# Optimization experiments

Measured on AMD Instinct MI355X. Metric: run time of the kernel, lower is better.

The kernel has to match this reference:

```python
import jax, jax.numpy as jnp
import numpy as np

B, T, N, C = 4, 6, 512, 8
HID, FEAT, EMB, IN_DIM = 64, 16, 32, 1
KS, KC, HORIZON = 3, 2, 3
ALPHA = 3.0

def _init(key, shape):
    fin = shape[-2] if len(shape) >= 2 else shape[-1]
    return jax.random.normal(key, shape, dtype=jnp.float32) * (1.0 / fin) ** 0.5

def setup_inputs():
    ks = jax.random.split(jax.random.key(0), 32)
    L_enc = (IN_DIM + FEAT + HID) * KS * KC
    L_dec = (HID + FEAT + HID) * KS * KC
    return {
        "X_seq": jax.random.normal(ks[0], (B, T, N, C), dtype=jnp.float32),
        "As": jax.random.uniform(ks[1], (N, N), dtype=jnp.float32) / N,
        "Ac": jax.random.uniform(ks[2], (C, C), dtype=jnp.float32) / C,
        "feature": jax.random.normal(ks[3], (N, FEAT), dtype=jnp.float32),
        "Wu_S": _init(ks[4], (C, HID)), "Wv_S": _init(ks[5], (C, HID)),
        "Wu_C": _init(ks[6], (N, HID)), "Wv_C": _init(ks[7], (N, HID)),
        "mfS_w1": _init(ks[8], (4, 2, 256)), "mfS_b1": jnp.zeros((4, 256), jnp.float32),
        "mfS_w2": _init(ks[9], (4, 256, 256)), "mfS_b2": jnp.zeros((4, 256), jnp.float32),
        "mfC_w1": _init(ks[10], (4, 2, 256)), "mfC_b1": jnp.zeros((4, 256), jnp.float32),
        "mfC_w2": _init(ks[11], (4, 256, 256)), "mfC_b2": jnp.zeros((4, 256), jnp.float32),
        "enc_gW": _init(ks[12], (L_enc, 2 * HID)), "enc_gb": jnp.zeros((2 * HID,), jnp.float32),
        "enc_cW": _init(ks[13], (L_enc, HID)), "enc_cb": jnp.zeros((HID,), jnp.float32),
        "dec_gW": _init(ks[14], (L_dec, 2 * HID)), "dec_gb": jnp.zeros((2 * HID,), jnp.float32),
        "dec_cW": _init(ks[15], (L_dec, HID)), "dec_cb": jnp.zeros((HID,), jnp.float32),
        "out_w1": _init(ks[16], (HID, EMB)), "out_b1": jnp.zeros((EMB,), jnp.float32),
        "out_w2": _init(ks[17], (EMB, IN_DIM)), "out_b2": jnp.zeros((IN_DIM,), jnp.float32),
    }

def _mlp(x, w1, b1, w2, b2):
    return jax.nn.relu(x @ w1 + b1) @ w2 + b2

def _mixed_fusion(A, P, w1, b1, w2, b2):
    # node_feat = [rowsum(A), rowsum(P)]; key/value MLPs indexed 0:key_A 1:key_P 2:val_A 3:val_P
    nf = jnp.stack([A.sum(-1), P.sum(-1)], axis=-1)            # [n, 2]
    An, Pn = A @ nf, P @ nf
    key = _mlp(An, w1[0], b1[0], w2[0], b2[0]) + _mlp(Pn, w1[1], b1[1], w2[1], b2[1])
    val = _mlp(An, w1[2], b1[2], w2[2], b2[2]) + _mlp(Pn, w1[3], b1[3], w2[3], b2[3])
    a = jax.nn.sigmoid(key @ val.T)
    return a * A + (1.0 - a) * P

def _adaptive_graph(Xf, Wu, Wv):
    U = jnp.tanh(ALPHA * Xf @ Wu)                              # [b,t,n,h]
    V = jnp.tanh(ALPHA * Xf @ Wv)
    M = jnp.einsum('btnh,btmh->nm', U, V)
    # Ps = softmax(relu(M - M^T)) matches einsum pair in torch source
    return jax.nn.softmax(jax.nn.relu(M - M.T), axis=-1)

def _cheby(G, K):
    mats = [jnp.eye(G.shape[0], dtype=G.dtype), G]
    for _ in range(2, K):
        mats.append(2.0 * G @ mats[-1] - mats[-2])
    return jnp.stack(mats[:K], axis=0)                         # [K, n, n]

def _bdg(X, Gs_set, Gc_set, W, b):
    # X: [b,n,c,l]; fused Ks x Kc Chebyshev mode products; cat order (k, j, l) matches torch cat
    t1 = jnp.einsum('bncl,knm->kbmcl', X, Gs_set)
    t2 = jnp.einsum('kbmcl,jcd->bmdkjl', t1, Gc_set)
    feat = t2.reshape(t2.shape[0], t2.shape[1], t2.shape[2], -1)
    return feat @ W + b

def _cell(Xt, Ht, featx, Gs_set, Gc_set, gW, gb, cW, cb):
    XH = jnp.concatenate([Xt, Ht, featx], axis=-1)
    uv = _bdg(XH, Gs_set, Gc_set, gW, gb)
    update = jax.nn.sigmoid(uv[..., :HID])
    reset = jax.nn.sigmoid(uv[..., HID:])
    cand_in = jnp.concatenate([Xt, reset * Ht, featx], axis=-1)
    cand = jnp.tanh(_bdg(cand_in, Gs_set, Gc_set, cW, cb))
    return (1.0 - update) * Ht + update * cand

def _forward(X_seq, As, Ac, feature, Wu_S, Wv_S, Wu_C, Wv_C,
             mfS_w1, mfS_b1, mfS_w2, mfS_b2, mfC_w1, mfC_b1, mfC_w2, mfC_b2,
             enc_gW, enc_gb, enc_cW, enc_cb, dec_gW, dec_gb, dec_cW, dec_cb,
             out_w1, out_b1, out_w2, out_b2):
    # MGP_Gen: adaptive spatial / categorical graphs fused with priors
    Ps = _adaptive_graph(X_seq, Wu_S, Wv_S)
    Gs = _mixed_fusion(As, Ps, mfS_w1, mfS_b1, mfS_w2, mfS_b2)
    Xc = jnp.swapaxes(X_seq, 2, 3)                             # [b,t,c,n]
    Pc = _adaptive_graph(Xc, Wu_C, Wv_C)
    Gc = _mixed_fusion(Ac, Pc, mfC_w1, mfC_b1, mfC_w2, mfC_b2)
    Gs_set, Gc_set = _cheby(Gs, KS), _cheby(Gc, KC)
    featx = jnp.broadcast_to(feature[None, :, None, :], (B, N, C, FEAT))
    X5 = X_seq[..., None]                                      # [b,t,n,c,1]
    Ht = jnp.zeros((B, N, C, HID), dtype=X_seq.dtype)
    for t in range(T):                                         # encoder GRU over history
        Ht = _cell(X5[:, t], Ht, featx, Gs_set, Gc_set, enc_gW, enc_gb, enc_cW, enc_cb)
    deco_in, Hd = Ht, Ht
    outs = []
    for _ in range(HORIZON):
        Hd = _cell(deco_in, Hd, featx, Gs_set, Gc_set, dec_gW, dec_gb, dec_cW, dec_cb)
        outs.append(_mlp(Hd, out_w1, out_b1, out_w2, out_b2))
        deco_in = Hd
    return jnp.stack(outs, axis=1)                             # [b, horizon, n, c, 1]

def reference(X_seq, As, Ac, feature, Wu_S, Wv_S, Wu_C, Wv_C, mfS_w1, mfS_b1, mfS_w2, mfS_b2, mfC_w1, mfC_b1, mfC_w2, mfC_b2, enc_gW, enc_gb, enc_cW, enc_cb, dec_gW, dec_gb, dec_cW, dec_cb, out_w1, out_b1, out_w2, out_b2):
    return _forward(X_seq, As, Ac, feature, Wu_S, Wv_S, Wu_C, Wv_C, mfS_w1, mfS_b1, mfS_w2, mfS_b2, mfC_w1, mfC_b1, mfC_w2, mfC_b2, enc_gW, enc_gb, enc_cW, enc_cb, dec_gW, dec_gb, dec_cW, dec_cb, out_w1, out_b1, out_w2, out_b2)
```

## Files before the change

### kernel.cpp

```cpp
#include <hip/hip_runtime.h>
#include <math.h>

constexpr int kB = 4, kT = 6, kN = 512, kC = 8;
constexpr int kH = 64, kF = 16, kE = 32;
constexpr int kKS = 3, kKC = 2, kHOR = 3;
constexpr int kBT = kB * kT;
constexpr int kRK = kBT * kH;
constexpr int L_ENC = 1 + kH + kF;
constexpr int L_DEC = kH + kH + kF;
constexpr int PL_ENC = 96;
constexpr int PL_DEC = 160;
constexpr int KP_ENC = 3 * PL_ENC;
constexpr int KP_DEC = 3 * PL_DEC;
constexpr float kALPHA = 3.0f;

typedef unsigned short ushortT;
typedef short short8 __attribute__((ext_vector_type(8)));
typedef float f32x4 __attribute__((ext_vector_type(4)));

__device__ __forceinline__ float sigm(float x) { return 1.0f / (1.0f + __expf(-x)); }

__device__ __forceinline__ ushortT f2bf(float f) {
    union { float f; unsigned int u; } v; v.f = f;
    unsigned int r = v.u + 0x7fffu + ((v.u >> 16) & 1u);
    return (ushortT)(r >> 16);
}

__device__ __forceinline__ void fma44(const float4& a, const float4& b, float acc[4][4]) {
    acc[0][0] += a.x*b.x; acc[0][1] += a.x*b.y; acc[0][2] += a.x*b.z; acc[0][3] += a.x*b.w;
    acc[1][0] += a.y*b.x; acc[1][1] += a.y*b.y; acc[1][2] += a.y*b.z; acc[1][3] += a.y*b.w;
    acc[2][0] += a.z*b.x; acc[2][1] += a.z*b.y; acc[2][2] += a.z*b.z; acc[2][3] += a.z*b.w;
    acc[3][0] += a.w*b.x; acc[3][1] += a.w*b.y; acc[3][2] += a.w*b.z; acc[3][3] += a.w*b.w;
}


__global__ __launch_bounds__(256) void k_uvproj_s(
    const float* __restrict__ X, const float* __restrict__ Wu, const float* __restrict__ Wv,
    float* __restrict__ Upr, float* __restrict__ Vpr)
{
    int idx = blockIdx.x * blockDim.x + threadIdx.x;
    if (idx >= kN * kBT * kH) return;
    int h = idx % kH; int bt = (idx / kH) % kBT; int n = idx / (kH * kBT);
    const float* xr = X + ((size_t)bt * kN + n) * kC;
    float u = 0.f, v = 0.f;
#pragma unroll
    for (int c = 0; c < kC; ++c) { float x = xr[c]; u += x * Wu[c*kH + h]; v += x * Wv[c*kH + h]; }
    Upr[(size_t)n * kRK + bt * kH + h] = tanhf(kALPHA * u);
    Vpr[(size_t)n * kRK + bt * kH + h] = tanhf(kALPHA * v);
}

__global__ __launch_bounds__(512) void k_uvproj_c2(
    const float* __restrict__ X, const float* __restrict__ WuC, const float* __restrict__ WvC,
    float* __restrict__ Uc, float* __restrict__ Vc)
{
    __shared__ float Xs[4096];
    __shared__ float Wus[4096], Wvs[4096];
    int bt = blockIdx.x, tid = threadIdx.x;
    for (int i = tid; i < 4096; i += 512) Xs[i] = X[(size_t)bt*4096 + i];
    int c = tid >> 6, h = tid & 63;
    float u = 0.f, v = 0.f;
    for (int n0 = 0; n0 < 512; n0 += 64) {
        __syncthreads();
        for (int i = tid; i < 4096; i += 512) { Wus[i] = WuC[n0*64 + i]; Wvs[i] = WvC[n0*64 + i]; }
        __syncthreads();
#pragma unroll 8
        for (int nn = 0; nn < 64; ++nn) {
            float x = Xs[(n0+nn)*8 + c];
// ... 178 lines not shown
    if (tid < 16) {
        int i = tid >> 1, comp = tid & 1;
        float an = 0.f, pn = 0.f;
#pragma unroll
        for (int j = 0; j < 8; ++j) {
            float nfj = comp ? 1.f : rsA[j];
            an += Ac[i*8+j] * nfj; pn += Pcs[i*8+j] * nfj;
        }
        Ans[i*2+comp] = an; Pns[i*2+comp] = pn;
    }
    __syncthreads();
    for (int e = tid; e < 2048; e += 256) {
        int i = e >> 8, o = e & 255;
        hA[i][o] = fmaxf(Ans[i*2]*w1[qa*512 + o] + Ans[i*2+1]*w1[qa*512 + 256 + o] + b1[qa*256 + o], 0.f);
        hP[i][o] = fmaxf(Pns[i*2]*w1[qp*512 + o] + Pns[i*2+1]*w1[qp*512 + 256 + o] + b1[qp*256 + o], 0.f);
    }
    __syncthreads();
    for (int e = tid; e < 512; e += 256) {
        int i = e >> 6, oc = c0 + (e & 63);
        float s = b2[qa*256 + oc] + b2[qp*256 + oc];
        for (int k = 0; k < 256; ++k)
            s += hA[i][k]*w2[(size_t)qa*65536 + k*256 + oc] + hP[i][k]*w2[(size_t)qp*65536 + k*256 + oc];
        keyval[(size_t)kv*2048 + i*256 + oc] = s;
    }
}

__global__ void k_gcfuse2(const float* __restrict__ keyval, const float* __restrict__ Mc,
                          const float* __restrict__ Ac, float* __restrict__ GcF)
{
    __shared__ float Pcs[64];
    int t = threadIdx.x; if (t >= 64) return;
    if (t < 8) {
        int i = t;
        float row[8]; float mx = -1e30f;
#pragma unroll
        for (int j = 0; j < 8; ++j) { float v = fmaxf(Mc[i*8+j] - Mc[j*8+i], 0.f); row[j] = v; mx = fmaxf(mx, v); }
        float s = 0.f;
#pragma unroll
        for (int j = 0; j < 8; ++j) { row[j] = __expf(row[j] - mx); s += row[j]; }
        float inv = 1.f / s;
#pragma unroll
        for (int j = 0; j < 8; ++j) Pcs[i*8+j] = row[j] * inv;
    }
    __syncthreads();
    int c = t >> 3, d = t & 7;
    const float* key = keyval;
    const float* val = keyval + 2048;
    float s = 0.f;
    for (int k = 0; k < 256; ++k) s += key[c*256 + k] * val[d*256 + k];
    float a = sigm(s);
    GcF[c*8 + d] = a*Ac[c*8 + d] + (1.f - a)*Pcs[c*8 + d];
}


__global__ void k_transp(const float* __restrict__ G, ushortT* __restrict__ Gt)
{
    __shared__ float tile[32][33];
    int bx = blockIdx.x * 32, by = blockIdx.y * 32;
    int x = threadIdx.x, y0 = threadIdx.y;
    for (int yy = y0; yy < 32; yy += 8) tile[yy][x] = G[(size_t)(by+yy)*kN + bx + x];
    __syncthreads();
    for (int yy = y0; yy < 32; yy += 8) Gt[(size_t)(bx+yy)*kN + by + x] = f2bf(tile[x][yy]);
}

__global__ __launch_bounds__(256) void k_prep_wt(
    const float* __restrict__ W, ushortT* __restrict__ WT,
    int L, int PL, int KP, int outW, int mode)
{
    int idx = blockIdx.x * blockDim.x + threadIdx.x;
    if (idx >= 2 * outW * KP) return;
    int qp = idx % KP, o = idx / KP;
    int kk = qp / PL, l = qp - kk * PL;
    int lo;
    if (mode == 1) lo = (l < 64) ? l + 1 : (l == 64) ? 0 : (l < 80) ? L : (l - 15);
    else lo = l;
    int j = o / outW, oo = o - j * outW;
    float v = (lo < L) ? W[(size_t)((kk*2 + j)*L + lo) * outW + oo] : 0.f;
    WT[idx] = f2bf(v);
}

__global__ __launch_bounds__(256) void k_cheby_mfma(
    const ushortT* __restrict__ Gst, ushortT* __restrict__ Gst2)
{
    __shared__ short sA[128][40];
    __shared__ short sB[128][40];
    int tid = threadIdx.x;
    int m0 = blockIdx.y * 128, j0 = blockIdx.x * 128;
    int w = tid >> 6, lane = tid & 63, wr = w >> 1, wc = w & 1;
    f32x4 acc[4][4];
#pragma unroll
    for (int i = 0; i < 4; ++i)
#pragma unroll
        for (int j = 0; j < 4; ++j) acc[i][j] = (f32x4){0.f, 0.f, 0.f, 0.f};
    for (int k0 = 0; k0 < kN; k0 += 32) {
        {
            int row = tid >> 1, lc = (tid & 1) * 16;
            const ushortT* p = Gst + (size_t)(m0 + row)*kN + k0 + lc;
            *(short8*)&sA[row][lc]     = *(const short8*)p;
            *(short8*)&sA[row][lc + 8] = *(const short8*)(p + 8);
        }
        {
            int kr = tid & 31, jc = (tid >> 5) * 8;
#pragma unroll
            for (int rep = 0; rep < 2; ++rep) {
                short8 v = *(const short8*)(Gst + (size_t)(k0 + kr)*kN + j0 + jc + rep*64);
#pragma unroll
                for (int i = 0; i < 8; ++i) sB[jc + rep*64 + i][kr] = v[i];
            }
        }
        __syncthreads();
        short8 af[4], bfr[4];
#pragma unroll
        for (int mi = 0; mi < 4; ++mi)
            af[mi] = *(const short8*)&sA[wr*64 + mi*16 + (lane & 15)][(lane >> 4) * 8];
#pragma unroll
        for (int ni = 0; ni < 4; ++ni)
            bfr[ni] = *(const short8*)&sB[wc*64 + ni*16 + (lane & 15)][(lane >> 4) * 8];
#pragma unroll
        for (int mi = 0; mi < 4; ++mi)
#pragma unroll
            for (int ni = 0; ni < 4; ++ni)
                acc[mi][ni] = __builtin_amdgcn_mfma_f32_16x16x32_bf16(af[mi], bfr[ni], acc[mi][ni], 0, 0, 0);
        __syncthreads();
    }
#pragma unroll
    for (int mi = 0; mi < 4; ++mi) {
#pragma unroll
        for (int ni = 0; ni < 4; ++ni) {
            int row0 = m0 + wr*64 + mi*16 + (lane >> 4) * 4;
            int col  = j0 + wc*64 + ni*16 + (lane & 15);
#pragma unroll
            for (int q = 0; q < 4; ++q) {
                int row = row0 + q;
                Gst2[(size_t)row*kN + col] = f2bf(2.f*acc[mi][ni][q] - (row == col ? 1.f : 0.f));
            }
        }
    }
}

template<int CLP, int PL, int ACTW, int OFF>
__global__ __launch_bounds__(256) void k_t1m(
    const ushortT* __restrict__ Gst, const ushortT* __restrict__ Xin, ushortT* __restrict__ Yout)
{
    __shared__ short sA[128][40];
    __shared__ short sB[128][40];
    int tid = threadIdx.x;
    int ki = blockIdx.z >> 2, b = blockIdx.z & 3;
    const ushortT* A = Gst + (size_t)ki * kN * kN;
    const ushortT* B = Xin + (size_t)b * kN * CLP;
    ushortT* C = Yout + (size_t)(ki*4 + b) * kN * CLP;
    int m0 = blockIdx.y * 128, j0 = blockIdx.x * 128;
    int w = tid >> 6, lane = tid & 63, wr = w >> 1, wc = w & 1;
    f32x4 acc[4][4];
#pragma unroll
    for (int i = 0; i < 4; ++i)
#pragma unroll
        for (int j = 0; j < 4; ++j) acc[i][j] = (f32x4){0.f, 0.f, 0.f, 0.f};

    for (int k0 = 0; k0 < kN; k0 += 32) {
        {
            int row = tid >> 1, lc = (tid & 1) * 16;
            const ushortT* p = A + (size_t)(m0 + row)*kN + k0 + lc;
            *(short8*)&sA[row][lc]     = *(const short8*)p;
            *(short8*)&sA[row][lc + 8] = *(const short8*)(p + 8);
        }
        {
            int kr = tid & 31, jc = (tid >> 5) * 8;
#pragma unroll
            for (int rep = 0; rep < 2; ++rep) {
                int j = j0 + jc + rep*64;
                int cg = j / ACTW;
                int col = cg*PL + OFF + (j - cg*ACTW);
                short8 v = *(const short8*)(B + (size_t)(k0 + kr)*CLP + col);
#pragma unroll
                for (int i = 0; i < 8; ++i) sB[jc + rep*64 + i][kr] = v[i];
            }
        }
        __syncthreads();
        short8 af[4], bfr[4];
#pragma unroll
        for (int mi = 0; mi < 4; ++mi)
            af[mi] = *(const short8*)&sA[wr*64 + mi*16 + (lane & 15)][(lane >> 4) * 8];
#pragma unroll
        for (int ni = 0; ni < 4; ++ni)
            bfr[ni] = *(const short8*)&sB[wc*64 + ni*16 + (lane & 15)][(lane >> 4) * 8];
#pragma unroll
        for (int mi = 0; mi < 4; ++mi)
#pragma unroll
            for (int ni = 0; ni < 4; ++ni)
                acc[mi][ni] = __builtin_amdgcn_mfma_f32_16x16x32_bf16(af[mi], bfr[ni], acc[mi][ni], 0, 0, 0);
        __syncthreads();
    }
#pragma unroll
    for (int mi = 0; mi < 4; ++mi) {
#pragma unroll
        for (int ni = 0; ni < 4; ++ni) {
            int row = m0 + wr*64 + mi*16 + (lane >> 4) * 4;
            int fj = j0 + wc*64 + ni*16;
            int cg = fj / ACTW;
            int col = cg*PL + OFF + (fj - cg*ACTW) + (lane & 15);
#pragma unroll
            for (int q = 0; q < 4; ++q)
                C[(size_t)(row + q)*CLP + col] = f2bf(acc[mi][ni][q]);
        }
    }
}

template<int PL, int KP, int XOFF>
__global__ __launch_bounds__(256) void k_gates_f(
    ushortT* __restrict__ XH, const ushortT* __restrict__ Yb,
    const ushortT* __restrict__ WT, const float* __restrict__ GcM,
    const float* __restrict__ gb, const float* __restrict__ Ht,
    float* __restrict__ upd)
{
    __shared__ short sA[64][40];
    __shared__ short sB[256][40];
    __shared__ float sEp[32][260];
    __shared__ float GcS[64], gbS[128];
    int tid = threadIdx.x;
    int r0 = blockIdx.x * 64;
    int b = r0 >> 12, rr = r0 & 4095;
    const ushortT* src0 = XH + (size_t)r0 * PL;
    const ushortT* src1 = Yb + ((size_t)b * 4096 + rr) * PL;
    const ushortT* src2 = Yb + ((size_t)(4 + b) * 4096 + rr) * PL;
    if (tid < 64) GcS[tid] = GcM[tid];
    if (tid >= 64 && tid < 192) gbS[tid - 64] = gb[tid - 64];
    int w = tid >> 6, lane = tid & 63;
    f32x4 acc[4][4];
#pragma unroll
    for (int i = 0; i < 4; ++i)
#pragma unroll
        for (int j = 0; j < 4; ++j) acc[i][j] = (f32x4){0.f, 0.f, 0.f, 0.f};

    for (int k0 = 0; k0 < KP; k0 += 32) {
        int kk = k0 / PL, l0 = k0 - kk * PL;
        const ushortT* Ap = (kk == 0) ? src0 : (kk == 1) ? src1 : src2;
        {
            int row = tid >> 2, lc = (tid & 3) * 8;
            *(short8*)&sA[row][lc] = *(const short8*)(Ap + (size_t)row*PL + l0 + lc);
        }
        {
            const ushortT* p = WT + (size_t)tid*KP + k0;
            *(short8*)&sB[tid][0]  = *(const short8*)(p);
            *(short8*)&sB[tid][8]  = *(const short8*)(p + 8);
            *(short8*)&sB[tid][16] = *(const short8*)(p + 16);
            *(short8*)&sB[tid][24] = *(const short8*)(p + 24);
        }
        __syncthreads();
        short8 af[4], bfr[4];
#pragma unroll
        for (int mi = 0; mi < 4; ++mi)
            af[mi] = *(const short8*)&sA[mi*16 + (lane & 15)][(lane >> 4) * 8];
#pragma unroll
        for (int ni = 0; ni < 4; ++ni)
            bfr[ni] = *(const short8*)&sB[w*64 + ni*16 + (lane & 15)][(lane >> 4) * 8];
#pragma unroll
        for (int mi = 0; mi < 4; ++mi)
#pragma unroll
            for (int ni = 0; ni < 4; ++ni)
                acc[mi][ni] = __builtin_amdgcn_mfma_f32_16x16x32_bf16(af[mi], bfr[ni], acc[mi][ni], 0, 0, 0);
        __syncthreads();
    }
    for (int chunk = 0; chunk < 2; ++chunk) {
#pragma unroll
        for (int mi2 = 0; mi2 < 2; ++mi2) {
            int mi = chunk*2 + mi2;
#pragma unroll
            for (int ni = 0; ni < 4; ++ni)
#pragma unroll
                for (int q = 0; q < 4; ++q)
                    sEp[mi2*16 + (lane >> 4)*4 + q][w*64 + ni*16 + (lane & 15)] = acc[mi][ni][q];
        }
        __syncthreads();
        for (int it = 0; it < 16; ++it) {
            int idx = it*256 + tid;
            int o = idx & 127, rloc = idx >> 7;
            int r = r0 + chunk*32 + rloc;
            int d = r & 7, bb = rloc & ~7;
            float pre = sEp[rloc][o] + gbS[o];
#pragma unroll
            for (int c = 0; c < 8; ++c) pre += GcS[c*8 + d] * sEp[bb + c][128 + o];
            float g = sigm(pre);
            if (o < 64) upd[(size_t)r*64 + o] = g;
            else {
                int h = o - 64;
                XH[(size_t)r*PL + XOFF + h] = f2bf(g * Ht[(size_t)r*64 + h]);
            }
        }
        __syncthreads();
    }
}

template<int PL, int KP>
__global__ __launch_bounds__(256) void k_cand_f(
    const ushortT* __restrict__ XH, const ushortT* __restrict__ Yb,
    const ushortT* __restrict__ WT, const float* __restrict__ GcM,
    const float* __restrict__ cb, const float* __restrict__ upd,
    float* __restrict__ Ht)
{
    __shared__ short sA[64][40];
    __shared__ short sB[128][40];
    __shared__ float sEp[64][132];
    __shared__ float GcS[64], cbS[64];
    int tid = threadIdx.x;
    int r0 = blockIdx.x * 64;
    int b = r0 >> 12, rr = r0 & 4095;
    const ushortT* src0 = XH + (size_t)r0 * PL;
    const ushortT* src1 = Yb + ((size_t)b * 4096 + rr) * PL;
    const ushortT* src2 = Yb + ((size_t)(4 + b) * 4096 + rr) * PL;
    if (tid < 64) GcS[tid] = GcM[tid];
    if (tid >= 64 && tid < 128) cbS[tid - 64] = cb[tid - 64];
    int w = tid >> 6, lane = tid & 63;
    f32x4 acc[4][2];
#pragma unroll
    for (int i = 0; i < 4; ++i)
#pragma unroll
        for (int j = 0; j < 2; ++j) acc[i][j] = (f32x4){0.f, 0.f, 0.f, 0.f};

    for (int k0 = 0; k0 < KP; k0 += 32) {
        int kk = k0 / PL, l0 = k0 - kk * PL;
        const ushortT* Ap = (kk == 0) ? src0 : (kk == 1) ? src1 : src2;
        {
            int row = tid >> 2, lc = (tid & 3) * 8;
            *(short8*)&sA[row][lc] = *(const short8*)(Ap + (size_t)row*PL + l0 + lc);
        }
        {
            int col = tid >> 1, seg = (tid & 1) * 16;
            const ushortT* p = WT + (size_t)col*KP + k0 + seg;
            *(short8*)&sB[col][seg]     = *(const short8*)p;
            *(short8*)&sB[col][seg + 8] = *(const short8*)(p + 8);
        }
        __syncthreads();
        short8 af[4], bfr[2];
#pragma unroll
        for (int mi = 0; mi < 4; ++mi)
            af[mi] = *(const short8*)&sA[mi*16 + (lane & 15)][(lane >> 4) * 8];
#pragma unroll
        for (int ni = 0; ni < 2; ++ni)
            bfr[ni] = *(const short8*)&sB[w*32 + ni*16 + (lane & 15)][(lane >> 4) * 8];
#pragma unroll
        for (int mi = 0; mi < 4; ++mi)
#pragma unroll
            for (int ni = 0; ni < 2; ++ni)
                acc[mi][ni] = __builtin_amdgcn_mfma_f32_16x16x32_bf16(af[mi], bfr[ni], acc[mi][ni], 0, 0, 0);
        __syncthreads();
    }
#pragma unroll
    for (int mi = 0; mi < 4; ++mi)
#pragma unroll
        for (int ni = 0; ni < 2; ++ni)
#pragma unroll
            for (int q = 0; q < 4; ++q)
                sEp[mi*16 + (lane >> 4)*4 + q][w*32 + ni*16 + (lane & 15)] = acc[mi][ni][q];
    __syncthreads();
    for (int it = 0; it < 16; ++it) {
        int idx = it*256 + tid;
        int o = idx & 63, rloc = idx >> 6;
        int r = r0 + rloc;
        int d = r & 7, bb = rloc & ~7;
        float pre = sEp[rloc][o] + cbS[o];
#pragma unroll
        for (int c = 0; c < 8; ++c) pre += GcS[c*8 + d] * sEp[bb + c][64 + o];
        float cv = tanhf(pre);
        float u = upd[(size_t)r*64 + o];
        float h0 = Ht[(size_t)r*64 + o];
        Ht[(size_t)r*64 + o] = (1.f - u)*h0 + u*cv;
    }
}


__global__ __launch_bounds__(256) void k_build_enc(
    const float* __restrict__ X, int t, const float* __restrict__ Ht,
    const float* __restrict__ featr, ushortT* __restrict__ XH)
{
    int idx = blockIdx.x * blockDim.x + threadIdx.x;
    if (idx >= 16384 * PL_ENC) return;
    int l = idx % PL_ENC; int r = idx / PL_ENC;
    int c = r & 7; int m = (r >> 3) & 511; int b = r >> 12;
    float v;
    if (l < 64)            v = Ht[(size_t)r*kH + l];
    else if (l == 64)      v = X[(((size_t)b*kT + t)*kN + m)*kC + c];
    else if (l < 80)       v = 0.f;
    else                   v = featr[m*kF + (l - 80)];
    XH[idx] = f2bf(v);
}

__global__ __launch_bounds__(256) void k_build_dec(
    const float* __restrict__ Ht, const float* __restrict__ featr, ushortT* __restrict__ XH)
{
    int idx = blockIdx.x * blockDim.x + threadIdx.x;
    if (idx >= 16384 * PL_DEC) return;
    int l = idx % PL_DEC; int r = idx / PL_DEC;
    int m = (r >> 3) & 511;
    float v;
    if (l < kH)            v = Ht[(size_t)r*kH + l];
    else if (l < 2*kH)     v = Ht[(size_t)r*kH + l - kH];
    else if (l < L_DEC)    v = featr[m*kF + l - 2*kH];
    else                   v = 0.f;
    XH[idx] = f2bf(v);
}

__global__ __launch_bounds__(256) void k_outmlp(
    const float* __restrict__ Hd, const float* __restrict__ w1, const float* __restrict__ b1,
    const float* __restrict__ w2, const float* __restrict__ b2, float* __restrict__ out, int hz)
{
    int idx = blockIdx.x * blockDim.x + threadIdx.x;
    if (idx >= kB*kN*kC) return;
    int c = idx % kC; int m = (idx / kC) % kN; int b = idx / (kC*kN);
    const float* h = Hd + (size_t)idx * kH;
    float hreg[kH];
#pragma unroll
    for (int k = 0; k < kH; ++k) hreg[k] = h[k];
    float acc = b2[0];
    for (int e = 0; e < kE; ++e) {
        float s = b1[e];
#pragma unroll
        for (int k = 0; k < kH; ++k) s += hreg[k] * w1[k*kE + e];
        acc += fmaxf(s, 0.f) * w2[e];
    }
    out[((size_t)(b*kHOR + hz)*kN + m)*kC + c] = acc;
}

extern "C" void kernel_launch(void* const* d_in, const int* in_sizes, int n_in,
                              void* d_out, int out_size, void* d_ws, size_t ws_size,
                              hipStream_t stream)
{
    (void)in_sizes; (void)n_in; (void)out_size; (void)ws_size;
    const float* X      = (const float*)d_in[0];
    const float* As     = (const float*)d_in[1];
    const float* Ac     = (const float*)d_in[2];
    const float* featr  = (const float*)d_in[3];
    const float* WuS    = (const float*)d_in[4];
    const float* WvS    = (const float*)d_in[5];
    const float* WuC    = (const float*)d_in[6];
    const float* WvC    = (const float*)d_in[7];
    const float* mfS_w1 = (const float*)d_in[8];
    const float* mfS_b1 = (const float*)d_in[9];
    const float* mfS_w2 = (const float*)d_in[10];
    const float* mfS_b2 = (const float*)d_in[11];
    const float* mfC_w1 = (const float*)d_in[12];
    const float* mfC_b1 = (const float*)d_in[13];
    const float* mfC_w2 = (const float*)d_in[14];
    const float* mfC_b2 = (const float*)d_in[15];
    const float* enc_gW = (const float*)d_in[16];
    const float* enc_gb = (const float*)d_in[17];
    const float* enc_cW = (const float*)d_in[18];
    const float* enc_cb = (const float*)d_in[19];
    const float* dec_gW = (const float*)d_in[20];
    const float* dec_gb = (const float*)d_in[21];
    const float* dec_cW = (const float*)d_in[22];
    const float* dec_cb = (const float*)d_in[23];
    const float* out_w1 = (const float*)d_in[24];
    const float* out_b1 = (const float*)d_in[25];
    const float* out_w2 = (const float*)d_in[26];
    const float* out_b2 = (const float*)d_in[27];
    float* out = (float*)d_out;
    float* ws = (float*)d_ws;

    float* Ht     = ws;
    float* updb   = Ht + 1048576;
    float* Gg     = updb + 1048576;
    float* Gs     = Gg + 4194304;
    float* smallf = Gs + 262144;
    float* nfS = smallf;
    float* AnS = nfS + 1024;
    float* PnS = AnS + 1024;
    float* McB = PnS + 1024;
    float* GcF = McB + 64;
    float* kvC = GcF + 64;
    ushortT* XHb  = (ushortT*)(smallf + 8192);
    ushortT* Yb   = XHb + 2621440;
    ushortT* GstB = Yb + 5242880;
    ushortT* WTg_e = GstB + 524288;
    ushortT* WTc_e = WTg_e + 73728;
    ushortT* WTg_d = WTc_e + 36864;
    ushortT* WTc_d = WTg_d + 122880;
    float* Upr   = Gg;
    float* Vpr   = Upr + 786432;
    float* part  = Vpr + 786432;
    float* Ms    = part + 1048576;
    float* Ps    = Ms + 262144;
    float* hidAP = Ps + 262144;
    float* keyS  = hidAP + 262144;
    float* valS  = keyS + 131072;
    float* w2tK  = valS + 131072;
    float* w2tV  = w2tK + 131072;
    float* Uc    = w2tV + 131072;
    float* Vc    = Uc + 12288;

    constexpr int CLP_ENC = kC * PL_ENC;
    constexpr int CLP_DEC = kC * PL_DEC;

    hipMemsetAsync(Ht, 0, (size_t)16384 * kH * sizeof(float), stream);

    k_prep_wt<<<(2*128*KP_ENC + 255)/256, 256, 0, stream>>>(enc_gW, WTg_e, L_ENC, PL_ENC, KP_ENC, 128, 1);
    k_prep_wt<<<(2*64 *KP_ENC + 255)/256, 256, 0, stream>>>(enc_cW, WTc_e, L_ENC, PL_ENC, KP_ENC, 64, 1);
    k_prep_wt<<<(2*128*KP_DEC + 255)/256, 256, 0, stream>>>(dec_gW, WTg_d, L_DEC, PL_DEC, KP_DEC, 128, 0);
    k_prep_wt<<<(2*64 *KP_DEC + 255)/256, 256, 0, stream>>>(dec_cW, WTc_d, L_DEC, PL_DEC, KP_DEC, 64, 0);
    k_prep_w2t<<<512, 256, 0, stream>>>(mfS_w2, w2tK, w2tV);

    k_uvproj_s<<<(kN*kBT*kH + 255)/256, 256, 0, stream>>>(X, WuS, WvS, Upr, Vpr);
    k_gemm_ntsk<<<dim3(8, 8, 4), 256, 0, stream>>>(Upr, Vpr, part, 512, 512, 1536, 384);
    k_redep<<<1024, 256, 0, stream>>>(part, 4, 262144, 512, Ms, 0, nullptr, nullptr);
    k_nfa<<<kN, 256, 0, stream>>>(As, nfS);
    k_softmax_anpn<<<kN, 256, 0, stream>>>(Ms, As, nfS, Ps, AnS, PnS);
    k_mlp1cat<<<1024, 256, 0, stream>>>(AnS, PnS, mfS_w1, mfS_b1, 0, 1, hidAP);
    k_gemm_ntsk<<<dim3(4, 8, 2), 256, 0, stream>>>(hidAP, w2tK, part, 512, 256, 512, 256);
    k_redep<<<512, 256, 0, stream>>>(part, 2, 131072, 256, keyS, 2, mfS_b2, mfS_b2 + 256);
    k_mlp1cat<<<1024, 256, 0, stream>>>(AnS, PnS, mfS_w1, mfS_b1, 2, 3, hidAP);
    k_gemm_ntsk<<<dim3(4, 8, 2), 256, 0, stream>>>(hidAP, w2tV, part, 512, 256, 512, 256);
    k_redep<<<512, 256, 0, stream>>>(part, 2, 131072, 256, valS, 2, mfS_b2 + 512, mfS_b2 + 768);
    k_gemm_ntsk<<<dim3(8, 8, 2), 256, 0, stream>>>(keyS, valS, part, 512, 512, 256, 128);
    k_redep<<<1024, 256, 0, stream>>>(part, 2, 262144, 512, Gs, 1, As, Ps);
    k_transp<<<dim3(16, 16), dim3(32, 8), 0, stream>>>(Gs, GstB);
    k_cheby_mfma<<<dim3(4, 4), 256, 0, stream>>>(GstB, GstB + 262144);

    k_uvproj_c2<<<kBT, 512, 0, stream>>>(X, WuC, WvC, Uc, Vc);
    k_mc2<<<1, 512, 0, stream>>>(Uc, Vc, McB);
    k_catmlp2<<<dim3(2, 4), 256, 0, stream>>>(McB, Ac, mfC_w1, mfC_b1, mfC_w2, mfC_b2, kvC);
    k_gcfuse2<<<1, 64, 0, stream>>>(kvC, McB, Ac, GcF);

    bool featDone = false;
    for (int t = 0; t < kT; ++t) {
        k_build_enc<<<(16384*PL_ENC + 255)/256, 256, 0, stream>>>(X, t, Ht, featr, XHb);
        if (!featDone) {
            k_t1m<CLP_ENC, PL_ENC, 16, 80><<<dim3(1, 4, 8), 256, 0, stream>>>(GstB, XHb, Yb);
            featDone = true;
        }
        k_t1m<CLP_ENC, PL_ENC, 80, 0><<<dim3(5, 4, 8), 256, 0, stream>>>(GstB, XHb, Yb);
        k_gates_f<PL_ENC, KP_ENC, 0><<<256, 256, 0, stream>>>(XHb, Yb, WTg_e, GcF, enc_gb, Ht, updb);
        k_t1m<CLP_ENC, PL_ENC, 64, 0><<<dim3(4, 4, 8), 256, 0, stream>>>(GstB, XHb, Yb);
        k_cand_f<PL_ENC, KP_ENC><<<256, 256, 0, stream>>>(XHb, Yb, WTc_e, GcF, enc_cb, updb, Ht);
    }

    featDone = false;
    for (int hz = 0; hz < kHOR; ++hz) {
        k_build_dec<<<(16384*PL_DEC + 255)/256, 256, 0, stream>>>(Ht, featr, XHb);
        if (!featDone) {
            k_t1m<CLP_DEC, PL_DEC, 16, 128><<<dim3(1, 4, 8), 256, 0, stream>>>(GstB, XHb, Yb);
            featDone = true;
        }
        k_t1m<CLP_DEC, PL_DEC, 128, 0><<<dim3(8, 4, 8), 256, 0, stream>>>(GstB, XHb, Yb);
        k_gates_f<PL_DEC, KP_DEC, 64><<<256, 256, 0, stream>>>(XHb, Yb, WTg_d, GcF, dec_gb, Ht, updb);
        k_t1m<CLP_DEC, PL_DEC, 64, 64><<<dim3(4, 4, 8), 256, 0, stream>>>(GstB, XHb, Yb);
        k_cand_f<PL_DEC, KP_DEC><<<256, 256, 0, stream>>>(XHb, Yb, WTc_d, GcF, dec_cb, updb, Ht);
        k_outmlp<<<(kB*kN*kC + 255)/256, 256, 0, stream>>>(Ht, out_w1, out_b1, out_w2, out_b2, out, hz);
    }
}
```

Baseline: 1.078 ms.

## Fuse GRU encoder/decoder loop into one persistent kernel with grid barriers

Replaces the per-step sequence of build, graph-matmul, gates, candidate and output-MLP launches with a single persistent kernel of 256 blocks. Stages are separated by a software grid barrier built on atomics. The separate input-building and output-MLP kernels are folded into the candidate epilogue, which writes the next step's bf16 inputs and the output directly. This removes many launch gaps and extra passes over memory. In exchange, the code now depends on all 256 blocks being co-resident, and the barrier spin-waits add their own latency.

```diff
diff --git a/kernel.cpp b/kernel.cpp
--- a/kernel.cpp
+++ b/kernel.cpp
@@ -13,6 +13,7 @@
 constexpr int KP_ENC = 3 * PL_ENC;
 constexpr int KP_DEC = 3 * PL_DEC;
 constexpr float kALPHA = 3.0f;
+constexpr int NB = 256;
 
 typedef unsigned short ushortT;
 typedef short short8 __attribute__((ext_vector_type(8)));
@@ -297,7 +298,6 @@
     GcF[c*8 + d] = a*Ac[c*8 + d] + (1.f - a)*Pcs[c*8 + d];
 }
 
-
 __global__ void k_transp(const float* __restrict__ G, ushortT* __restrict__ Gt)
 {
     __shared__ float tile[32][33];
@@ -383,19 +383,46 @@
     }
 }
 
-template<int CLP, int PL, int ACTW, int OFF>
-__global__ __launch_bounds__(256) void k_t1m(
-    const ushortT* __restrict__ Gst, const ushortT* __restrict__ Xin, ushortT* __restrict__ Yout)
-{
-    __shared__ short sA[128][40];
-    __shared__ short sB[128][40];
-    int tid = threadIdx.x;
-    int ki = blockIdx.z >> 2, b = blockIdx.z & 3;
-    const ushortT* A = Gst + (size_t)ki * kN * kN;
+
+union GruSmem {
+    struct { short A[128][40]; short B[128][40]; } t1;
+    struct { short A[64][40]; short B[256][40]; float Ep[32][260]; float Gc[64]; float gb[128]; } gt;
+    struct { short A[64][40]; short B[128][40]; float Ep[64][132]; float Hn[64][66]; float Out[64][4]; float Gc[64]; float cb[64]; } cd;
+};
+
+__device__ __forceinline__ void gridbar(int* arrive, int* gen, int g) {
+    __syncthreads();
+    if (threadIdx.x == 0) {
+        __threadfence();
+        int a = __hip_atomic_fetch_add(arrive, 1, __ATOMIC_ACQ_REL, __HIP_MEMORY_SCOPE_AGENT);
+        if (a == NB - 1) {
+            __hip_atomic_store(arrive, 0, __ATOMIC_RELAXED, __HIP_MEMORY_SCOPE_AGENT);
+            __hip_atomic_store(gen, g, __ATOMIC_RELEASE, __HIP_MEMORY_SCOPE_AGENT);
+        } else {
+            while (__hip_atomic_load(gen, __ATOMIC_ACQUIRE, __HIP_MEMORY_SCOPE_AGENT) < g)
+                __builtin_amdgcn_s_sleep(2);
+        }
+        __threadfence();
+    }
+    __syncthreads();
+}
+
+__device__ void t1_dev(GruSmem* sm, int tile,
+                       const ushortT* __restrict__ Gst, const ushortT* __restrict__ Xin,
+                       ushortT* __restrict__ Yout, int CLP, int PL, int ACTW, int OFF, int nct)
+{
+    int x = tile % nct; int rest = tile / nct; int y = rest & 3; int z = rest >> 2;
+    int ki = z >> 2, b = z & 3;
+    const ushortT* A = Gst + (size_t)ki * (kN * kN);
     const ushortT* B = Xin + (size_t)b * kN * CLP;
     ushortT* C = Yout + (size_t)(ki*4 + b) * kN * CLP;
-    int m0 = blockIdx.y * 128, j0 = blockIdx.x * 128;
+    int m0 = y * 128, j0 = x * 128;
+    int tid = threadIdx.x;
     int w = tid >> 6, lane = tid & 63, wr = w >> 1, wc = w & 1;
+    int kr = tid & 31, jc = (tid >> 5) * 8;
+    int colr0, colr1;
+    { int j = j0 + jc;      int cg = j / ACTW; colr0 = cg*PL + OFF + (j - cg*ACTW); }
+    { int j = j0 + jc + 64; int cg = j / ACTW; colr1 = cg*PL + OFF + (j - cg*ACTW); }
     f32x4 acc[4][4];
 #pragma unroll
     for (int i = 0; i < 4; ++i)
@@ -406,29 +433,25 @@
         {
             int row = tid >> 1, lc = (tid & 1) * 16;
             const ushortT* p = A + (size_t)(m0 + row)*kN + k0 + lc;
-            *(short8*)&sA[row][lc]     = *(const short8*)p;
-            *(short8*)&sA[row][lc + 8] = *(const short8*)(p + 8);
+            *(short8*)&sm->t1.A[row][lc]     = *(const short8*)p;
+            *(short8*)&sm->t1.A[row][lc + 8] = *(const short8*)(p + 8);
         }
         {
-            int kr = tid & 31, jc = (tid >> 5) * 8;
-#pragma unroll
-            for (int rep = 0; rep < 2; ++rep) {
-                int j = j0 + jc + rep*64;
-                int cg = j / ACTW;
-                int col = cg*PL + OFF + (j - cg*ACTW);
-                short8 v = *(const short8*)(B + (size_t)(k0 + kr)*CLP + col);
-#pragma unroll
-                for (int i = 0; i < 8; ++i) sB[jc + rep*64 + i][kr] = v[i];
-            }
+            short8 v0 = *(const short8*)(B + (size_t)(k0 + kr)*CLP + colr0);
+            short8 v1 = *(const short8*)(B + (size_t)(k0 + kr)*CLP + colr1);
+#pragma unroll
+            for (int i = 0; i < 8; ++i) sm->t1.B[jc + i][kr] = v0[i];
+#pragma unroll
+            for (int i = 0; i < 8; ++i) sm->t1.B[jc + 64 + i][kr] = v1[i];
         }
         __syncthreads();
         short8 af[4], bfr[4];
 #pragma unroll
         for (int mi = 0; mi < 4; ++mi)
-            af[mi] = *(const short8*)&sA[wr*64 + mi*16 + (lane & 15)][(lane >> 4) * 8];
+            af[mi] = *(const short8*)&sm->t1.A[wr*64 + mi*16 + (lane & 15)][(lane >> 4) * 8];
 #pragma unroll
         for (int ni = 0; ni < 4; ++ni)
-            bfr[ni] = *(const short8*)&sB[wc*64 + ni*16 + (lane & 15)][(lane >> 4) * 8];
+            bfr[ni] = *(const short8*)&sm->t1.B[wc*64 + ni*16 + (lane & 15)][(lane >> 4) * 8];
 #pragma unroll
         for (int mi = 0; mi < 4; ++mi)
 #pragma unroll
@@ -451,25 +474,18 @@
     }
 }
 
-template<int PL, int KP, int XOFF>
-__global__ __launch_bounds__(256) void k_gates_f(
-    ushortT* __restrict__ XH, const ushortT* __restrict__ Yb,
-    const ushortT* __restrict__ WT, const float* __restrict__ GcM,
-    const float* __restrict__ gb, const float* __restrict__ Ht,
-    float* __restrict__ upd)
-{
-    __shared__ short sA[64][40];
-    __shared__ short sB[256][40];
-    __shared__ float sEp[32][260];
-    __shared__ float GcS[64], gbS[128];
+__device__ void gates_dev(GruSmem* sm, int r0,
+    ushortT* __restrict__ XH, const ushortT* __restrict__ Yb, const ushortT* __restrict__ WT,
+    const float* __restrict__ GcM, const float* __restrict__ gb,
+    const float* __restrict__ Ht, float* __restrict__ upd, int PL, int KP, int XOFF)
+{
     int tid = threadIdx.x;
-    int r0 = blockIdx.x * 64;
     int b = r0 >> 12, rr = r0 & 4095;
     const ushortT* src0 = XH + (size_t)r0 * PL;
     const ushortT* src1 = Yb + ((size_t)b * 4096 + rr) * PL;
     const ushortT* src2 = Yb + ((size_t)(4 + b) * 4096 + rr) * PL;
-    if (tid < 64) GcS[tid] = GcM[tid];
-    if (tid >= 64 && tid < 192) gbS[tid - 64] = gb[tid - 64];
+    if (tid < 64) sm->gt.Gc[tid] = GcM[tid];
+    if (tid >= 64 && tid < 192) sm->gt.gb[tid - 64] = gb[tid - 64];
     int w = tid >> 6, lane = tid & 63;
     f32x4 acc[4][4];
 #pragma unroll
@@ -477,34 +493,36 @@
 #pragma unroll
         for (int j = 0; j < 4; ++j) acc[i][j] = (f32x4){0.f, 0.f, 0.f, 0.f};
 
+    int kk = 0, l0 = 0;
     for (int k0 = 0; k0 < KP; k0 += 32) {
-        int kk = k0 / PL, l0 = k0 - kk * PL;
         const ushortT* Ap = (kk == 0) ? src0 : (kk == 1) ? src1 : src2;
         {
             int row = tid >> 2, lc = (tid & 3) * 8;
-            *(short8*)&sA[row][lc] = *(const short8*)(Ap + (size_t)row*PL + l0 + lc);
+            *(short8*)&sm->gt.A[row][lc] = *(const short8*)(Ap + (size_t)row*PL + l0 + lc);
         }
         {
             const ushortT* p = WT + (size_t)tid*KP + k0;
-            *(short8*)&sB[tid][0]  = *(const short8*)(p);
-            *(short8*)&sB[tid][8]  = *(const short8*)(p + 8);
-            *(short8*)&sB[tid][16] = *(const short8*)(p + 16);
-            *(short8*)&sB[tid][24] = *(const short8*)(p + 24);
+            *(short8*)&sm->gt.B[tid][0]  = *(const short8*)(p);
+            *(short8*)&sm->gt.B[tid][8]  = *(const short8*)(p + 8);
+            *(short8*)&sm->gt.B[tid][16] = *(const short8*)(p + 16);
+            *(short8*)&sm->gt.B[tid][24] = *(const short8*)(p + 24);
         }
         __syncthreads();
         short8 af[4], bfr[4];
 #pragma unroll
         for (int mi = 0; mi < 4; ++mi)
-            af[mi] = *(const short8*)&sA[mi*16 + (lane & 15)][(lane >> 4) * 8];
+            af[mi] = *(const short8*)&sm->gt.A[mi*16 + (lane & 15)][(lane >> 4) * 8];
 #pragma unroll
         for (int ni = 0; ni < 4; ++ni)
-            bfr[ni] = *(const short8*)&sB[w*64 + ni*16 + (lane & 15)][(lane >> 4) * 8];
+            bfr[ni] = *(const short8*)&sm->gt.B[w*64 + ni*16 + (lane & 15)][(lane >> 4) * 8];
 #pragma unroll
         for (int mi = 0; mi < 4; ++mi)
 #pragma unroll
             for (int ni = 0; ni < 4; ++ni)
                 acc[mi][ni] = __builtin_amdgcn_mfma_f32_16x16x32_bf16(af[mi], bfr[ni], acc[mi][ni], 0, 0, 0);
         __syncthreads();
+        l0 += 32;
+        if (l0 >= PL) { ++kk; l0 = 0; }
     }
     for (int chunk = 0; chunk < 2; ++chunk) {
 #pragma unroll
@@ -514,7 +532,7 @@
             for (int ni = 0; ni < 4; ++ni)
 #pragma unroll
                 for (int q = 0; q < 4; ++q)
-                    sEp[mi2*16 + (lane >> 4)*4 + q][w*64 + ni*16 + (lane & 15)] = acc[mi][ni][q];
+                    sm->gt.Ep[mi2*16 + (lane >> 4)*4 + q][w*64 + ni*16 + (lane & 15)] = acc[mi][ni][q];
         }
         __syncthreads();
         for (int it = 0; it < 16; ++it) {
@@ -522,9 +540,9 @@
             int o = idx & 127, rloc = idx >> 7;
             int r = r0 + chunk*32 + rloc;
             int d = r & 7, bb = rloc & ~7;
-            float pre = sEp[rloc][o] + gbS[o];
-#pragma unroll
-            for (int c = 0; c < 8; ++c) pre += GcS[c*8 + d] * sEp[bb + c][128 + o];
+            float pre = sm->gt.Ep[rloc][o] + sm->gt.gb[o];
+#pragma unroll
+            for (int c = 0; c < 8; ++c) pre += sm->gt.Gc[c*8 + d] * sm->gt.Ep[bb + c][128 + o];
             float g = sigm(pre);
             if (o < 64) upd[(size_t)r*64 + o] = g;
             else {
@@ -536,25 +554,23 @@
     }
 }
 
-template<int PL, int KP>
-__global__ __launch_bounds__(256) void k_cand_f(
-    const ushortT* __restrict__ XH, const ushortT* __restrict__ Yb,
-    const ushortT* __restrict__ WT, const float* __restrict__ GcM,
-    const float* __restrict__ cb, const float* __restrict__ upd,
-    float* __restrict__ Ht)
-{
-    __shared__ short sA[64][40];
-    __shared__ short sB[128][40];
-    __shared__ float sEp[64][132];
-    __shared__ float GcS[64], cbS[64];
+__device__ void cand_dev(GruSmem* sm, int r0,
+    const ushortT* __restrict__ XH, const ushortT* __restrict__ Yb, const ushortT* __restrict__ WT,
+    const float* __restrict__ GcM, const float* __restrict__ cb,
+    const float* __restrict__ upd, float* __restrict__ Ht,
+    int PL, int KP, int mode, int tnext, const float* __restrict__ X,
+    ushortT* __restrict__ XHe, ushortT* __restrict__ XHd,
+    const float* __restrict__ ow1, const float* __restrict__ ob1,
+    const float* __restrict__ ow2, const float* __restrict__ ob2,
+    float* __restrict__ out, int hz)
+{
     int tid = threadIdx.x;
-    int r0 = blockIdx.x * 64;
     int b = r0 >> 12, rr = r0 & 4095;
     const ushortT* src0 = XH + (size_t)r0 * PL;
     const ushortT* src1 = Yb + ((size_t)b * 4096 + rr) * PL;
     const ushortT* src2 = Yb + ((size_t)(4 + b) * 4096 + rr) * PL;
-    if (tid < 64) GcS[tid] = GcM[tid];
-    if (tid >= 64 && tid < 128) cbS[tid - 64] = cb[tid - 64];
+    if (tid < 64) sm->cd.Gc[tid] = GcM[tid];
+    if (tid >= 64 && tid < 128) sm->cd.cb[tid - 64] = cb[tid - 64];
     int w = tid >> 6, lane = tid & 63;
     f32x4 acc[4][2];
 #pragma unroll
@@ -562,33 +578,35 @@
 #pragma unroll
         for (int j = 0; j < 2; ++j) acc[i][j] = (f32x4){0.f, 0.f, 0.f, 0.f};
 
+    int kk = 0, l0 = 0;
     for (int k0 = 0; k0 < KP; k0 += 32) {
-        int kk = k0 / PL, l0 = k0 - kk * PL;
         const ushortT* Ap = (kk == 0) ? src0 : (kk == 1) ? src1 : src2;
         {
             int row = tid >> 2, lc = (tid & 3) * 8;
-            *(short8*)&sA[row][lc] = *(const short8*)(Ap + (size_t)row*PL + l0 + lc);
+            *(short8*)&sm->cd.A[row][lc] = *(const short8*)(Ap + (size_t)row*PL + l0 + lc);
         }
         {
             int col = tid >> 1, seg = (tid & 1) * 16;
             const ushortT* p = WT + (size_t)col*KP + k0 + seg;
-            *(short8*)&sB[col][seg]     = *(const short8*)p;
-            *(short8*)&sB[col][seg + 8] = *(const short8*)(p + 8);
+            *(short8*)&sm->cd.B[col][seg]     = *(const short8*)p;
+            *(short8*)&sm->cd.B[col][seg + 8] = *(const short8*)(p + 8);
         }
         __syncthreads();
         short8 af[4], bfr[2];
 #pragma unroll
         for (int mi = 0; mi < 4; ++mi)
-            af[mi] = *(const short8*)&sA[mi*16 + (lane & 15)][(lane >> 4) * 8];
+            af[mi] = *(const short8*)&sm->cd.A[mi*16 + (lane & 15)][(lane >> 4) * 8];
 #pragma unroll
         for (int ni = 0; ni < 2; ++ni)
-            bfr[ni] = *(const short8*)&sB[w*32 + ni*16 + (lane & 15)][(lane >> 4) * 8];
+            bfr[ni] = *(const short8*)&sm->cd.B[w*32 + ni*16 + (lane & 15)][(lane >> 4) * 8];
 #pragma unroll
         for (int mi = 0; mi < 4; ++mi)
 #pragma unroll
             for (int ni = 0; ni < 2; ++ni)
                 acc[mi][ni] = __builtin_amdgcn_mfma_f32_16x16x32_bf16(af[mi], bfr[ni], acc[mi][ni], 0, 0, 0);
         __syncthreads();
+        l0 += 32;
+        if (l0 >= PL) { ++kk; l0 = 0; }
     }
 #pragma unroll
     for (int mi = 0; mi < 4; ++mi)
@@ -596,74 +614,134 @@
         for (int ni = 0; ni < 2; ++ni)
 #pragma unroll
             for (int q = 0; q < 4; ++q)
-                sEp[mi*16 + (lane >> 4)*4 + q][w*32 + ni*16 + (lane & 15)] = acc[mi][ni][q];
+                sm->cd.Ep[mi*16 + (lane >> 4)*4 + q][w*32 + ni*16 + (lane & 15)] = acc[mi][ni][q];
     __syncthreads();
     for (int it = 0; it < 16; ++it) {
         int idx = it*256 + tid;
         int o = idx & 63, rloc = idx >> 6;
         int r = r0 + rloc;
         int d = r & 7, bb = rloc & ~7;
-        float pre = sEp[rloc][o] + cbS[o];
-#pragma unroll
-        for (int c = 0; c < 8; ++c) pre += GcS[c*8 + d] * sEp[bb + c][64 + o];
+        float pre = sm->cd.Ep[rloc][o] + sm->cd.cb[o];
+#pragma unroll
+        for (int c = 0; c < 8; ++c) pre += sm->cd.Gc[c*8 + d] * sm->cd.Ep[bb + c][64 + o];
         float cv = tanhf(pre);
         float u = upd[(size_t)r*64 + o];
         float h0 = Ht[(size_t)r*64 + o];
-        Ht[(size_t)r*64 + o] = (1.f - u)*h0 + u*cv;
-    }
-}
-
-
-__global__ __launch_bounds__(256) void k_build_enc(
-    const float* __restrict__ X, int t, const float* __restrict__ Ht,
-    const float* __restrict__ featr, ushortT* __restrict__ XH)
-{
-    int idx = blockIdx.x * blockDim.x + threadIdx.x;
-    if (idx >= 16384 * PL_ENC) return;
-    int l = idx % PL_ENC; int r = idx / PL_ENC;
-    int c = r & 7; int m = (r >> 3) & 511; int b = r >> 12;
-    float v;
-    if (l < 64)            v = Ht[(size_t)r*kH + l];
-    else if (l == 64)      v = X[(((size_t)b*kT + t)*kN + m)*kC + c];
-    else if (l < 80)       v = 0.f;
-    else                   v = featr[m*kF + (l - 80)];
-    XH[idx] = f2bf(v);
-}
-
-__global__ __launch_bounds__(256) void k_build_dec(
-    const float* __restrict__ Ht, const float* __restrict__ featr, ushortT* __restrict__ XH)
-{
-    int idx = blockIdx.x * blockDim.x + threadIdx.x;
-    if (idx >= 16384 * PL_DEC) return;
-    int l = idx % PL_DEC; int r = idx / PL_DEC;
-    int m = (r >> 3) & 511;
-    float v;
-    if (l < kH)            v = Ht[(size_t)r*kH + l];
-    else if (l < 2*kH)     v = Ht[(size_t)r*kH + l - kH];
-    else if (l < L_DEC)    v = featr[m*kF + l - 2*kH];
-    else                   v = 0.f;
-    XH[idx] = f2bf(v);
-}
-
-__global__ __launch_bounds__(256) void k_outmlp(
-    const float* __restrict__ Hd, const float* __restrict__ w1, const float* __restrict__ b1,
-    const float* __restrict__ w2, const float* __restrict__ b2, float* __restrict__ out, int hz)
-{
-    int idx = blockIdx.x * blockDim.x + threadIdx.x;
-    if (idx >= kB*kN*kC) return;
-    int c = idx % kC; int m = (idx / kC) % kN; int b = idx / (kC*kN);
-    const float* h = Hd + (size_t)idx * kH;
-    float hreg[kH];
-#pragma unroll
-    for (int k = 0; k < kH; ++k) hreg[k] = h[k];
-    float acc = b2[0];
-    for (int e = 0; e < kE; ++e) {
-        float s = b1[e];
-#pragma unroll
-        for (int k = 0; k < kH; ++k) s += hreg[k] * w1[k*kE + e];
-        acc += fmaxf(s, 0.f) * w2[e];
-    }
-    out[((size_t)(b*kHOR + hz)*kN + m)*kC + c] = acc;
+        float hn = (1.f - u)*h0 + u*cv;
+        Ht[(size_t)r*64 + o] = hn;
+        sm->cd.Hn[rloc][o] = hn;
+        ushortT hb = f2bf(hn);
+        if (mode == 0) {
+            XHe[(size_t)r*PL_ENC + o] = hb;
+            if (o == 0) {
+                int c2 = r & 7, m = (r >> 3) & 511, b2 = r >> 12;
+                XHe[(size_t)r*PL_ENC + 64] = f2bf(X[(((size_t)b2*kT + tnext)*kN + m)*kC + c2]);
+            }
+        } else if (mode == 1 || mode == 2) {
+            XHd[(size_t)r*PL_DEC + o] = hb;
+            XHd[(size_t)r*PL_DEC + 64 + o] = hb;
+        }
+    }
+    if (mode >= 2) {
+        __syncthreads();
+        int row = tid >> 2, part = tid & 3;
+        float pe = 0.f;
+        for (int e = part*8; e < part*8 + 8; ++e) {
+            float s = ob1[e];
+#pragma unroll
+            for (int k = 0; k < kH; ++k) s += sm->cd.Hn[row][k] * ow1[k*kE + e];
+            pe += fmaxf(s, 0.f) * ow2[e];
+        }
+        sm->cd.Out[row][part] = pe;
+        __syncthreads();
+        if (tid < 64) {
+            int r = r0 + tid;
+            int c2 = r & 7, m = (r >> 3) & 511, b2 = r >> 12;
+            float v = ob2[0] + sm->cd.Out[tid][0] + sm->cd.Out[tid][1] + sm->cd.Out[tid][2] + sm->cd.Out[tid][3];
+            out[((size_t)(b2*kHOR + hz)*kN + m)*kC + c2] = v;
+        }
+        __syncthreads();
+    }
+}
+
+__global__ void __launch_bounds__(256) k_gru_persist(
+    const float* __restrict__ X, const float* __restrict__ featr,
+    const ushortT* __restrict__ Gst, ushortT* __restrict__ XHe, ushortT* __restrict__ XHd,
+    ushortT* __restrict__ Yb,
+    const ushortT* __restrict__ WTg_e, const ushortT* __restrict__ WTc_e,
+    const ushortT* __restrict__ WTg_d, const ushortT* __restrict__ WTc_d,
+    const float* __restrict__ GcF,
+    const float* __restrict__ egb, const float* __restrict__ ecb,
+    const float* __restrict__ dgb, const float* __restrict__ dcb,
+    float* __restrict__ Ht, float* __restrict__ upd,
+    const float* __restrict__ ow1, const float* __restrict__ ob1,
+    const float* __restrict__ ow2, const float* __restrict__ ob2,
+    float* __restrict__ out, int* __restrict__ bar)
+{
+    __shared__ GruSmem sm;
+    int blk = blockIdx.x, tid = threadIdx.x;
+    int g = 0;
+
+    for (int idx = blk*256 + tid; idx < 16384*PL_ENC; idx += NB*256) {
+        int l = idx % PL_ENC; int r = idx / PL_ENC;
+        float v;
+        if (l < 64) v = 0.f;
+        else if (l == 64) { int c = r & 7, m = (r >> 3) & 511, b = r >> 12; v = X[(((size_t)b*kT)*kN + m)*kC + c]; }
+        else if (l < 80) v = 0.f;
+        else { int m = (r >> 3) & 511; v = featr[m*kF + (l - 80)]; }
+        XHe[idx] = f2bf(v);
+    }
+    for (int idx = blk*256 + tid; idx < 16384*32; idx += NB*256) {
+        int l2 = idx & 31; int r = idx >> 5;
+        float v = (l2 < 16) ? featr[((r >> 3) & 511)*kF + l2] : 0.f;
+        XHd[(size_t)r*PL_DEC + 128 + l2] = f2bf(v);
+    }
+    for (int idx = blk*256 + tid; idx < 16384*64; idx += NB*256) Ht[idx] = 0.f;
+    ++g; gridbar(&bar[0], &bar[1], g);
+
+    for (int tile = blk; tile < 32; tile += NB)
+        t1_dev(&sm, tile, Gst, XHe, Yb, 768, PL_ENC, 16, 80, 1);
+    ++g; gridbar(&bar[0], &bar[1], g);
+
+#pragma clang loop unroll(disable)
+    for (int t = 0; t < kT; ++t) {
+        for (int tile = blk; tile < 160; tile += NB)
+            t1_dev(&sm, tile, Gst, XHe, Yb, 768, PL_ENC, 80, 0, 5);
+        ++g; gridbar(&bar[0], &bar[1], g);
+        for (int tile = blk; tile < 256; tile += NB)
+            gates_dev(&sm, tile*64, XHe, Yb, WTg_e, GcF, egb, Ht, upd, PL_ENC, KP_ENC, 0);
+        ++g; gridbar(&bar[0], &bar[1], g);
+        for (int tile = blk; tile < 128; tile += NB)
+            t1_dev(&sm, tile, Gst, XHe, Yb, 768, PL_ENC, 64, 0, 4);
+        ++g; gridbar(&bar[0], &bar[1], g);
+        int mode = (t < kT - 1) ? 0 : 1;
+        for (int tile = blk; tile < 256; tile += NB)
+            cand_dev(&sm, tile*64, XHe, Yb, WTc_e, GcF, ecb, upd, Ht, PL_ENC, KP_ENC,
+                     mode, t + 1, X, XHe, XHd, ow1, ob1, ow2, ob2, out, 0);
+        ++g; gridbar(&bar[0], &bar[1], g);
+    }
+
+    for (int tile = blk; tile < 32; tile += NB)
+        t1_dev(&sm, tile, Gst, XHd, Yb, 1280, PL_DEC, 16, 128, 1);
+    ++g; gridbar(&bar[0], &bar[1], g);
+
+#pragma clang loop unroll(disable)
+    for (int hz = 0; hz < kHOR; ++hz) {
+        for (int tile = blk; tile < 256; tile += NB)
+            t1_dev(&sm, tile, Gst, XHd, Yb, 1280, PL_DEC, 128, 0, 8);
+        ++g; gridbar(&bar[0], &bar[1], g);
+        for (int tile = blk; tile < 256; tile += NB)
+            gates_dev(&sm, tile*64, XHd, Yb, WTg_d, GcF, dgb, Ht, upd, PL_DEC, KP_DEC, 64);
+        ++g; gridbar(&bar[0], &bar[1], g);
+        for (int tile = blk; tile < 128; tile += NB)
+            t1_dev(&sm, tile, Gst, XHd, Yb, 1280, PL_DEC, 64, 64, 4);
+        ++g; gridbar(&bar[0], &bar[1], g);
+        int mode = (hz < kHOR - 1) ? 2 : 3;
+        for (int tile = blk; tile < 256; tile += NB)
+            cand_dev(&sm, tile*64, XHd, Yb, WTc_d, GcF, dcb, upd, Ht, PL_DEC, KP_DEC,
+                     mode, 0, X, XHe, XHd, ow1, ob1, ow2, ob2, out, hz);
+        if (hz < kHOR - 1) { ++g; gridbar(&bar[0], &bar[1], g); }
+    }
 }
 
 extern "C" void kernel_launch(void* const* d_in, const int* in_sizes, int n_in,
@@ -713,6 +791,7 @@
     float* McB = PnS + 1024;
     float* GcF = McB + 64;
     float* kvC = GcF + 64;
+    int*   bar = (int*)(kvC + 4096);
     ushortT* XHb  = (ushortT*)(smallf + 8192);
     ushortT* Yb   = XHb + 2621440;
     ushortT* GstB = Yb + 5242880;
@@ -720,6 +799,7 @@
     ushortT* WTc_e = WTg_e + 73728;
     ushortT* WTg_d = WTc_e + 36864;
     ushortT* WTc_d = WTg_d + 122880;
+    ushortT* XHd   = WTc_d + 61440;
     float* Upr   = Gg;
     float* Vpr   = Upr + 786432;
     float* part  = Vpr + 786432;
@@ -733,10 +813,7 @@
     float* Uc    = w2tV + 131072;
     float* Vc    = Uc + 12288;
 
-    constexpr int CLP_ENC = kC * PL_ENC;
-    constexpr int CLP_DEC = kC * PL_DEC;
-
-    hipMemsetAsync(Ht, 0, (size_t)16384 * kH * sizeof(float), stream);
+    hipMemsetAsync(bar, 0, 2*sizeof(int), stream);
 
     k_prep_wt<<<(2*128*KP_ENC + 255)/256, 256, 0, stream>>>(enc_gW, WTg_e, L_ENC, PL_ENC, KP_ENC, 128, 1);
     k_prep_wt<<<(2*64 *KP_ENC + 255)/256, 256, 0, stream>>>(enc_cW, WTc_e, L_ENC, PL_ENC, KP_ENC, 64, 1);
@@ -765,30 +842,9 @@
     k_catmlp2<<<dim3(2, 4), 256, 0, stream>>>(McB, Ac, mfC_w1, mfC_b1, mfC_w2, mfC_b2, kvC);
     k_gcfuse2<<<1, 64, 0, stream>>>(kvC, McB, Ac, GcF);
 
-    bool featDone = false;
-    for (int t = 0; t < kT; ++t) {
-        k_build_enc<<<(16384*PL_ENC + 255)/256, 256, 0, stream>>>(X, t, Ht, featr, XHb);
-        if (!featDone) {
-            k_t1m<CLP_ENC, PL_ENC, 16, 80><<<dim3(1, 4, 8), 256, 0, stream>>>(GstB, XHb, Yb);
-            featDone = true;
-        }
-        k_t1m<CLP_ENC, PL_ENC, 80, 0><<<dim3(5, 4, 8), 256, 0, stream>>>(GstB, XHb, Yb);
-        k_gates_f<PL_ENC, KP_ENC, 0><<<256, 256, 0, stream>>>(XHb, Yb, WTg_e, GcF, enc_gb, Ht, updb);
-        k_t1m<CLP_ENC, PL_ENC, 64, 0><<<dim3(4, 4, 8), 256, 0, stream>>>(GstB, XHb, Yb);
-        k_cand_f<PL_ENC, KP_ENC><<<256, 256, 0, stream>>>(XHb, Yb, WTc_e, GcF, enc_cb, updb, Ht);
-    }
-
-    featDone = false;
-    for (int hz = 0; hz < kHOR; ++hz) {
-        k_build_dec<<<(16384*PL_DEC + 255)/256, 256, 0, stream>>>(Ht, featr, XHb);
-        if (!featDone) {
-            k_t1m<CLP_DEC, PL_DEC, 16, 128><<<dim3(1, 4, 8), 256, 0, stream>>>(GstB, XHb, Yb);
-            featDone = true;
-        }
-        k_t1m<CLP_DEC, PL_DEC, 128, 0><<<dim3(8, 4, 8), 256, 0, stream>>>(GstB, XHb, Yb);
-        k_gates_f<PL_DEC, KP_DEC, 64><<<256, 256, 0, stream>>>(XHb, Yb, WTg_d, GcF, dec_gb, Ht, updb);
-        k_t1m<CLP_DEC, PL_DEC, 64, 64><<<dim3(4, 4, 8), 256, 0, stream>>>(GstB, XHb, Yb);
-        k_cand_f<PL_DEC, KP_DEC><<<256, 256, 0, stream>>>(XHb, Yb, WTc_d, GcF, dec_cb, updb, Ht);
-        k_outmlp<<<(kB*kN*kC + 255)/256, 256, 0, stream>>>(Ht, out_w1, out_b1, out_w2, out_b2, out, hz);
-    }
-}
+    k_gru_persist<<<NB, 256, 0, stream>>>(
+        X, featr, GstB, XHb, XHd, Yb,
+        WTg_e, WTc_e, WTg_d, WTc_d,
+        GcF, enc_gb, enc_cb, dec_gb, dec_cb,
+        Ht, updb, out_w1, out_b1, out_w2, out_b2, out, bar);
+}
```

Result: slower. 3.204 ms (+197.3%).
